# Kernel optimization log

Measured on AMD Instinct MI355X. Metric: run time of the kernel, lower is better.

The kernel has to match this reference:

```python
import jax, jax.numpy as jnp
import numpy as np

B, CIN, L, D, H, DK, DV, K, KE = 8, 16, 256, 256, 8, 32, 32, 3, 5
EPS = 1e-9

def r2c(p):
    return p[..., 0] + 1j * p[..., 1]

def c2r(z):
    return jnp.stack([jnp.real(z), jnp.imag(z)], axis=-1)

def conv1d(x, w):
    # x: [B,C,L] complex, w: [O,C,Kt] complex, 'same' padding (pad = K//2)
    kt = w.shape[-1]; pad = kt // 2; Lx = x.shape[-1]
    xp = jnp.pad(x, ((0, 0), (0, 0), (pad, pad)))
    return sum(jnp.einsum('bcl,oc->bol', xp[:, :, i:i + Lx], w[:, :, i]) for i in range(kt))

def eca(x, w):
    # Efficient Channel Attention (complex): global avg pool over length,
    # 1D conv (kernel KE) across channels, split sigmoid gate, rescale.
    C = x.shape[1]; pad = w.shape[0] // 2
    y = x.mean(axis=-1)                              # [B,C] complex
    yp = jnp.pad(y, ((0, 0), (pad, pad)))
    z = sum(w[i] * yp[:, i:i + C] for i in range(w.shape[0]))
    a = jax.nn.sigmoid(z.real) + 1j * jax.nn.sigmoid(z.imag)
    return x * a[:, :, None]

def magminmax(s):
    # MagMinMaxNorm: min-max normalize magnitudes along last dim, keep phase.
    mag = jnp.abs(s)
    mn = mag.min(axis=-1, keepdims=True)
    mx = mag.max(axis=-1, keepdims=True)
    return s * (((mag - mn) / (mx - mn + EPS)) / (mag + EPS))

def mha(qi, ki, vi, Wq, Wk, Wv, Wo):
    # qi/ki/vi: [B, L, D] complex
    b, lq, _ = qi.shape
    q = jnp.einsum('bld,de->ble', qi, Wq).reshape(b, lq, H, DK)
    k = jnp.einsum('bld,de->ble', ki, Wk).reshape(b, -1, H, DK)
    v = jnp.einsum('bld,de->ble', vi, Wv).reshape(b, -1, H, DV)
    s = jnp.einsum('bqhd,bkhd->bhqk', q, k) * (1.0 / DK ** 0.5)
    o = jnp.einsum('bhqk,bkhd->bqhd', magminmax(s), v).reshape(b, lq, H * DV)
    return jnp.einsum('ble,ed->bld', o, Wo)

def ssca(A, Bx, Wq, Wk, Wv, Wo, eca_w, conv_w):
    # A, Bx: [B, D, L] complex. Wq/Wk/Wv/Wo indexed [AA, BB, AB, BA].
    At = jnp.swapaxes(A, 1, 2)
    Bt = jnp.swapaxes(Bx, 1, 2)
    Waa = mha(At, At, At, Wq[0], Wk[0], Wv[0], Wo[0])
    Xbb = mha(Bt, Bt, Bt, Wq[1], Wk[1], Wv[1], Wo[1])
    Yab = mha(At, Bt, Bt, Wq[2], Wk[2], Wv[2], Wo[2])
    Zba = mha(Bt, At, At, Wq[3], Wk[3], Wv[3], Wo[3])
    # cat along sequence dim (dim=1 pre-transpose in torch), then back to [B, D, 4L]
    Xc = jnp.swapaxes(jnp.concatenate([Waa, Xbb, Yab, Zba], axis=1), 1, 2)
    return conv1d(eca(Xc, eca_w), conv_w)

def fusion(X1, X2, head_w, head_b, wq, wk, wv, wo, ssca_eca_w, ssca_conv_w, top_eca_w):
    X1c, X2c = r2c(X1), r2c(X2)
    hw, hb = r2c(head_w), r2c(head_b)
    Wq, Wk, Wv, Wo = r2c(wq), r2c(wk), r2c(wv), r2c(wo)
    se, sc, te = r2c(ssca_eca_w), r2c(ssca_conv_w), r2c(top_eca_w)
    A = conv1d(X1c, hw[0]) + hb[0][None, :, None]
    Bc = conv1d(X2c, hw[1]) + hb[1][None, :, None]
    R = ssca(A, Bc, Wq[0], Wk[0], Wv[0], Wo[0], se[0], sc[0])
    kk = ssca(jnp.fft.ifft(A, axis=-1), jnp.fft.ifft(Bc, axis=-1),
              Wq[1], Wk[1], Wv[1], Wo[1], se[1], sc[1])
    R2 = jnp.concatenate([R, jnp.fft.fft(kk, axis=-1)], axis=1)      # [B, 2D, 4L]
    k2 = jnp.concatenate([kk, jnp.fft.ifft(R2[:, :D], axis=-1)], axis=1)
    return eca(R2, te[0]), eca(k2, te[1])

def setup_inputs() -> dict:
    key = jax.random.key(0)
    ks = jax.random.split(key, 11)
    def rn(k, shape, s=1.0):
        return jax.random.normal(k, shape, dtype=jnp.float32) * s
    wscale = 1.0 / D ** 0.5
    return {
        'X1': rn(ks[0], (B, CIN, L, 2)),
        'X2': rn(ks[1], (B, CIN, L, 2)),
        'head_w': rn(ks[2], (2, D, CIN, K, 2), 0.1),
        'head_b': rn(ks[3], (2, D, 2), 0.1),
        'wq': rn(ks[4], (2, 4, D, H * DK, 2), wscale),
        'wk': rn(ks[5], (2, 4, D, H * DK, 2), wscale),
        'wv': rn(ks[6], (2, 4, D, H * DV, 2), wscale),
        'wo': rn(ks[7], (2, 4, H * DV, D, 2), wscale),
        'ssca_eca_w': rn(ks[8], (2, KE, 2), 0.3),
        'ssca_conv_w': rn(ks[9], (2, D, D, K, 2), wscale),
        'top_eca_w': rn(ks[10], (2, KE, 2), 0.3),
    }

def reference(X1, X2, head_w, head_b, wq, wk, wv, wo, ssca_eca_w, ssca_conv_w, top_eca_w):
    Rc, kc = fusion(X1, X2, head_w, head_b, wq, wk, wv, wo, ssca_eca_w, ssca_conv_w, top_eca_w)
    return c2r(Rc), c2r(kc)
```

## Files before the change

kernel.cpp:

```cpp
#include <hip/hip_runtime.h>
#include <math.h>

namespace {

constexpr int Bn = 8, CINn = 16, Ln = 256, Dn = 256, Hn = 8, DKn = 32, DVn = 32;
constexpr int KWn = 3, KEn = 5, L4n = 1024;
constexpr float EPSf = 1e-9f;
constexpr int XP = 1040;
constexpr int LP = 40;

typedef __attribute__((ext_vector_type(8))) short short8b;
typedef __attribute__((ext_vector_type(4))) float f32x4;

__device__ __forceinline__ float2 cmul(float2 a, float2 b){
  return make_float2(a.x*b.x - a.y*b.y, a.x*b.y + a.y*b.x);
}
__device__ __forceinline__ float2 cfma(float2 a, float2 b, float2 c){
  c.x = fmaf(a.x, b.x, c.x); c.x = fmaf(-a.y, b.y, c.x);
  c.y = fmaf(a.x, b.y, c.y); c.y = fmaf(a.y, b.x, c.y);
  return c;
}
__device__ __forceinline__ ushort f2bf(float f){
  uint u = __float_as_uint(f);
  u += 0x7fffu + ((u >> 16) & 1u);
  return (ushort)(u >> 16);
}
__device__ __forceinline__ short8b neg8(short8b v){
  union { short8b s; uint u[4]; } x; x.s = v;
  #pragma unroll
  for (int i = 0; i < 4; ++i) x.u[i] ^= 0x80008000u;
  return x.s;
}

__global__ void head_conv_kernel(const float2* __restrict__ X, const float2* __restrict__ hw,
                                 const float2* __restrict__ hb, float2* __restrict__ out){
  int idx = blockIdx.x * blockDim.x + threadIdx.x;
  if (idx >= Bn*Dn*Ln) return;
  int l = idx & (Ln-1);
  int o = (idx >> 8) & (Dn-1);
  int b = idx >> 16;
  float2 acc = hb[o];
  for (int c = 0; c < CINn; ++c){
    const float2* xr = X + (size_t)(b*CINn + c)*Ln;
    const float2* wr = hw + (size_t)(o*CINn + c)*KWn;
    #pragma unroll
    for (int i = 0; i < KWn; ++i){
      int ll = l + i - 1;
      if (ll >= 0 && ll < Ln) acc = cfma(xr[ll], wr[i], acc);
    }
  }
  out[idx] = acc;
}

template<int N, int LOG>
__global__ void fft_rows_kernel(const float2* __restrict__ src0, float2* __restrict__ dst0,
                                int schans, int scoff, int dchans, int dcoff,
                                float sign, float scale){
  __shared__ float2 buf[N];
  __shared__ float2 tw[N/2];
  int row = blockIdx.x;
  int rb = row >> 8, rc = row & 255;
  const float2* src = src0 + (size_t)(rb*schans + scoff + rc)*N;
  float2* dst = dst0 + (size_t)(rb*dchans + dcoff + rc)*N;
  int tid = threadIdx.x;
  for (int i = tid; i < N/2; i += 256){
    float a = sign * 6.2831853071795864f * (float)i / (float)N;
    float s, c; __sincosf(a, &s, &c);
    tw[i] = make_float2(c, s);
  }
  for (int i = tid; i < N; i += 256){
    unsigned r = __brev((unsigned)i) >> (32 - LOG);
    buf[r] = src[i];
  }
  __syncthreads();
  for (int st = 1; st <= LOG; ++st){
    int half = 1 << (st-1);
    for (int bf = tid; bf < N/2; bf += 256){
      int blk = bf >> (st-1);
      int pos = bf & (half-1);
      int i0 = (blk << st) + pos;
      int i1 = i0 + half;
      float2 w = tw[pos << (LOG-st)];
      float2 u = buf[i0];
      float2 t = cmul(w, buf[i1]);
      buf[i0] = make_float2(u.x + t.x, u.y + t.y);
      buf[i1] = make_float2(u.x - t.x, u.y - t.y);
    }
    __syncthreads();
  }
  for (int i = tid; i < N; i += 256)
    dst[i] = make_float2(buf[i].x * scale, buf[i].y * scale);
}

__device__ __forceinline__ void cgemm_core(
    const ushort* __restrict__ Are, const ushort* __restrict__ Aim, int pitchA, int am0,
    const ushort* __restrict__ Bre, const ushort* __restrict__ Bim, int pitchB, int n0,
    int K, int conv, float2* __restrict__ cbase, size_t crow, int cmode,
    ushort* __restrict__ ore, ushort* __restrict__ oim)
{
  __shared__ ushort sh[10240];
  ushort* As_re = sh;
  ushort* As_im = sh + 2560;
  ushort* Bs_re = sh + 5120;
  ushort* Bs_im = sh + 7680;
  int tid = threadIdx.x;
  int lane = tid & 63, w = tid >> 6;
  int wm = w >> 1, wn = w & 1;
  int lrow = lane & 15, lhalf = lane >> 4;
  f32x4 ar[2][2], ai[2][2];
  #pragma unroll
  for (int s = 0; s < 2; ++s)
    #pragma unroll
    for (int t = 0; t < 2; ++t){ ar[s][t] = (f32x4){0,0,0,0}; ai[s][t] = (f32x4){0,0,0,0}; }
  int nk = K >> 5;
  for (int kc = 0; kc < nk; ++kc){
    int k0 = kc << 5;
    __syncthreads();
    #pragma unroll
    for (int rep = 0; rep < 2; ++rep){
      int q = tid + rep*256;
      int row = q >> 3, kq = (q & 7)*4;
      size_t go = (size_t)(am0 + row)*pitchA + k0 + kq;
      *(uint2*)&As_re[row*LP + kq] = *(const uint2*)&Are[go];
      *(uint2*)&As_im[row*LP + kq] = *(const uint2*)&Aim[go];
    }
    if (!conv){
      #pragma unroll
      for (int rep = 0; rep < 2; ++rep){
        int q = tid + rep*256;
        int k = q >> 4, nq = (q & 15)*4;
        size_t go = (size_t)(k0 + k)*pitchB + n0 + nq;
        uint2 vr = *(const uint2*)&Bre[go];
        uint2 vi = *(const uint2*)&Bim[go];
        ushort* dr = &Bs_re[nq*LP + k];
        ushort* di = &Bs_im[nq*LP + k];
        dr[0]    = (ushort)(vr.x);      di[0]    = (ushort)(vi.x);
        dr[LP]   = (ushort)(vr.x>>16);  di[LP]   = (ushort)(vi.x>>16);
        dr[2*LP] = (ushort)(vr.y);      di[2*LP] = (ushort)(vi.y);
        dr[3*LP] = (ushort)(vr.y>>16);  di[3*LP] = (ushort)(vi.y>>16);
      }
    } else {
      #pragma unroll
      for (int rep = 0; rep < 8; ++rep){
        int idx = tid + rep*256;
        int k = idx >> 6, nn = idx & 63;
        uint kk = (uint)(k0 + k);
        uint c = (kk * 0xAAABu) >> 17;
        int i = (int)(kk - c*3u);
        size_t go = (size_t)c*XP + 8 + n0 + nn + i - 1;
        Bs_re[nn*LP + k] = Bre[go];
        Bs_im[nn*LP + k] = Bim[go];
      }
    }
    __syncthreads();
    short8b afr[2], afi[2], bfr[2], bfi[2];
    #pragma unroll
    for (int s = 0; s < 2; ++s){
      int row = wm*32 + s*16 + lrow;
      afr[s] = *(const short8b*)&As_re[row*LP + lhalf*8];
      afi[s] = *(const short8b*)&As_im[row*LP + lhalf*8];
    }
    #pragma unroll
    for (int t = 0; t < 2; ++t){
      int row = wn*32 + t*16 + lrow;
      bfr[t] = *(const short8b*)&Bs_re[row*LP + lhalf*8];
      bfi[t] = *(const short8b*)&Bs_im[row*LP + lhalf*8];
    }
    #pragma unroll
    for (int s = 0; s < 2; ++s){
      short8b ain = neg8(afi[s]);
      #pragma unroll
      for (int t = 0; t < 2; ++t){
        ar[s][t] = __builtin_amdgcn_mfma_f32_16x16x32_bf16(ain,    bfi[t], ar[s][t], 0, 0, 0);
        ar[s][t] = __builtin_amdgcn_mfma_f32_16x16x32_bf16(afr[s], bfr[t], ar[s][t], 0, 0, 0);
        ai[s][t] = __builtin_amdgcn_mfma_f32_16x16x32_bf16(afi[s], bfr[t], ai[s][t], 0, 0, 0);
        ai[s][t] = __builtin_amdgcn_mfma_f32_16x16x32_bf16(afr[s], bfi[t], ai[s][t], 0, 0, 0);
      }
    }
  }
  if (cmode == 0){
    #pragma unroll
    for (int s = 0; s < 2; ++s)
      #pragma unroll
      for (int t = 0; t < 2; ++t)
        #pragma unroll
        for (int r = 0; r < 4; ++r){
          int mm = wm*32 + s*16 + lhalf*4 + r;
          int nn = wn*32 + t*16 + lrow;
          if (ore){
            ore[(size_t)mm*crow + nn] = f2bf(ar[s][t][r]);
            oim[(size_t)mm*crow + nn] = f2bf(ai[s][t][r]);
          } else {
            cbase[(size_t)mm*crow + nn] = make_float2(ar[s][t][r], ai[s][t][r]);
          }
        }
  } else {
    float2* T = (float2*)sh;
    #pragma unroll
    for (int h2 = 0; h2 < 2; ++h2){
      __syncthreads();
      if (wn == h2){
        #pragma unroll
        for (int s = 0; s < 2; ++s)
          #pragma unroll
          for (int t = 0; t < 2; ++t)
            #pragma unroll
            for (int r = 0; r < 4; ++r){
              int mm = wm*32 + s*16 + lhalf*4 + r;
              int nn = t*16 + lrow;
              T[mm*33 + nn] = make_float2(ar[s][t][r], ai[s][t][r]);
            }
      }
      __syncthreads();
      #pragma unroll
      for (int rep = 0; rep < 8; ++rep){
        int idx = tid + rep*256;
        int mm = idx & 63, nn = idx >> 6;
        float2 v = T[mm*33 + nn];
        if (ore){
          ore[(size_t)(h2*32 + nn)*crow + mm] = f2bf(v.x);
          oim[(size_t)(h2*32 + nn)*crow + mm] = f2bf(v.y);
        } else {
          cbase[(size_t)(h2*32 + nn)*crow + mm] = v;
        }
      }
    }
  }
}

__global__ __launch_bounds__(256) void qkv_mfma(
    const ushort* __restrict__ aAre, const ushort* __restrict__ aAim,
    const ushort* __restrict__ aBre, const ushort* __restrict__ aBim,
    const ushort* __restrict__ WqRe, const ushort* __restrict__ WqIm,
    const ushort* __restrict__ WkRe, const ushort* __restrict__ WkIm,
    const ushort* __restrict__ WvRe, const ushort* __restrict__ WvIm,
    ushort* __restrict__ QpRe, ushort* __restrict__ QpIm,
    ushort* __restrict__ KpRe, ushort* __restrict__ KpIm,
    ushort* __restrict__ VpRe, ushort* __restrict__ VpIm,
    int set, int m0, size_t pstride)
{
  int my = blockIdx.y;
  int ml = my / 3, which = my - ml*3;
  int m = m0 + ml;
  bool useA = (which == 0) ? (m == 0 || m == 2) : (m == 0 || m == 3);
  const ushort* Are = useA ? aAre : aBre;
  const ushort* Aim = useA ? aAim : aBim;
  const ushort* WRe = (which == 0) ? WqRe : (which == 1) ? WkRe : WvRe;
  const ushort* WIm = (which == 0) ? WqIm : (which == 1) ? WkIm : WvIm;
  size_t woff = (size_t)(set*4 + m)*Dn*Dn;
  int bx = blockIdx.x;
  int nt = bx & 3, mt = (bx >> 2) & 3, b = bx >> 4;
  int l0 = mt*64, e0 = nt*64;
  const ushort* ARe = Are + (size_t)b*Ln*Dn;
  const ushort* AIm = Aim + (size_t)b*Ln*Dn;
  size_t po = (size_t)ml*pstride;
  if (which == 2){
    ushort* orp = VpRe + po + ((size_t)b*Dn + e0)*Ln + l0;
    ushort* oip = VpIm + po + ((size_t)b*Dn + e0)*Ln + l0;
    cgemm_core(ARe, AIm, Dn, l0, WRe + woff, WIm + woff, Dn, e0, Dn, 0,
               nullptr, Ln, 1, orp, oip);
  } else {
    ushort* orp = ((which == 0) ? QpRe : KpRe) + po + ((size_t)b*Ln + l0)*Dn + e0;
    ushort* oip = ((which == 0) ? QpIm : KpIm) + po + ((size_t)b*Ln + l0)*Dn + e0;
    cgemm_core(ARe, AIm, Dn, l0, WRe + woff, WIm + woff, Dn, e0, Dn, 0,
               nullptr, Dn, 0, orp, oip);
  }
}

__global__ __launch_bounds__(256) void wo_mfma(
    const ushort* __restrict__ ORe, const ushort* __restrict__ OIm,
    const ushort* __restrict__ WoRe, const ushort* __restrict__ WoIm,
    float2* __restrict__ Xc, int set, int m0)
{
  int ml = blockIdx.y;
  int m = m0 + ml;
  size_t woff = (size_t)(set*4 + m)*Dn*Dn;
  int bx = blockIdx.x;
  int nt = bx & 3, mt = (bx >> 2) & 3, b = bx >> 4;
  int l0 = mt*64, d0 = nt*64;
  const ushort* ARe = ORe + ((size_t)ml*Bn + b)*Ln*Dn;
  const ushort* AIm = OIm + ((size_t)ml*Bn + b)*Ln*Dn;
  float2* cb = Xc + ((size_t)b*Dn + d0)*L4n + m*Ln + l0;
  cgemm_core(ARe, AIm, Dn, l0, WoRe + woff, WoIm + woff, Dn, d0, Dn, 0,
             cb, L4n, 1, nullptr, nullptr);
}

__global__ __launch_bounds__(256) void conv_mfma(
    const ushort* __restrict__ WRe, const ushort* __restrict__ WIm,
    const ushort* __restrict__ XRe, const ushort* __restrict__ XIm,
    float2* __restrict__ out, int ochans)
{
  int bx = blockIdx.x;
  int xt = bx & 15, ot = (bx >> 4) & 3, b = bx >> 6;
  int o0 = ot*64, x0 = xt*64;
  const ushort* xr = XRe + (size_t)b*Dn*XP;
  const ushort* xi = XIm + (size_t)b*Dn*XP;
  float2* cb = out + ((size_t)(b*ochans) + o0)*L4n + x0;
  cgemm_core(WRe, WIm, 768, o0, xr, xi, XP, x0, 768, 1, cb, L4n, 0,
             nullptr, nullptr);
}

__global__ __launch_bounds__(256) void attn_mfma(
    const ushort* __restrict__ QRe, const ushort* __restrict__ QIm,
    const ushort* __restrict__ KRe, const ushort* __restrict__ KIm,
    const ushort* __restrict__ VRe, const ushort* __restrict__ VIm,
    ushort* __restrict__ ORe, ushort* __restrict__ OIm, size_t pstride)
{
  size_t po = (size_t)blockIdx.y*pstride;
  const ushort* qre = QRe + po; const ushort* qim = QIm + po;
  const ushort* kre = KRe + po; const ushort* kim = KIm + po;
  const ushort* vre = VRe + po; const ushort* vim = VIm + po;
  ushort* ore = ORe + po; ushort* oim = OIm + po;
  int bx = blockIdx.x;
  int qt = bx >> 6, h = (bx >> 3) & 7, b = bx & 7;
  int q0 = qt*16;
  int tid = threadIdx.x;
  int lane = tid & 63, w = tid >> 6;
  int lg = lane >> 4, lr = lane & 15;
  __shared__ ushort PsRe[16*264];
  __shared__ ushort PsIm[16*264];
  __shared__ float2 mmb[4][4][4];
  __shared__ float2 red[4][16][32];
  const float scl = 0.17677669529663687f;

  size_t qoff = ((size_t)(b*Ln + q0 + lr))*Dn + h*DKn + lg*8;
  short8b aqr = *(const short8b*)&qre[qoff];
  short8b aqi = *(const short8b*)&qim[qoff];
  short8b aqin = neg8(aqi);

  f32x4 sr[4], si[4];
  #pragma unroll
  for (int t = 0; t < 4; ++t){ sr[t] = (f32x4){0,0,0,0}; si[t] = (f32x4){0,0,0,0}; }
  #pragma unroll
  for (int t = 0; t < 4; ++t){
    int kcol = w*64 + t*16 + lr;
    size_t koff = ((size_t)(b*Ln + kcol))*Dn + h*DKn + lg*8;
    short8b bkr = *(const short8b*)&kre[koff];
    short8b bki = *(const short8b*)&kim[koff];
    sr[t] = __builtin_amdgcn_mfma_f32_16x16x32_bf16(aqin, bki, sr[t], 0, 0, 0);
    sr[t] = __builtin_amdgcn_mfma_f32_16x16x32_bf16(aqr,  bkr, sr[t], 0, 0, 0);
    si[t] = __builtin_amdgcn_mfma_f32_16x16x32_bf16(aqi,  bkr, si[t], 0, 0, 0);
    si[t] = __builtin_amdgcn_mfma_f32_16x16x32_bf16(aqr,  bki, si[t], 0, 0, 0);
  }
  float mag[4][4];
  float mnr[4], mxr[4];
  #pragma unroll
  for (int r = 0; r < 4; ++r){ mnr[r] = 3.4e38f; mxr[r] = 0.f; }
  #pragma unroll
  for (int t = 0; t < 4; ++t)
    #pragma unroll
    for (int r = 0; r < 4; ++r){
      float x = sr[t][r]*scl, y = si[t][r]*scl;
      sr[t][r] = x; si[t][r] = y;
      float m = sqrtf(x*x + y*y);
      mag[t][r] = m;
      mnr[r] = fminf(mnr[r], m); mxr[r] = fmaxf(mxr[r], m);
    }
  #pragma unroll
  for (int off = 1; off < 16; off <<= 1)
    #pragma unroll
    for (int r = 0; r < 4; ++r){
      mnr[r] = fminf(mnr[r], __shfl_xor(mnr[r], off));
      mxr[r] = fmaxf(mxr[r], __shfl_xor(mxr[r], off));
    }
  if (lr == 0){
    #pragma unroll
    for (int r = 0; r < 4; ++r) mmb[w][lg][r] = make_float2(mnr[r], mxr[r]);
  }
  __syncthreads();
  float fmn[4], fmx[4];
  #pragma unroll
  for (int r = 0; r < 4; ++r){
    float2 v0 = mmb[0][lg][r], v1 = mmb[1][lg][r];
    float2 v2 = mmb[2][lg][r], v3 = mmb[3][lg][r];
    fmn[r] = fminf(fminf(v0.x, v1.x), fminf(v2.x, v3.x));
    fmx[r] = fmaxf(fmaxf(v0.y, v1.y), fmaxf(v2.y, v3.y));
  }
  #pragma unroll
  for (int t = 0; t < 4; ++t)
    #pragma unroll
    for (int r = 0; r < 4; ++r){
      int q = lg*4 + r, k = w*64 + t*16 + lr;
      float m = mag[t][r];
      float f = ((m - fmn[r]) / (fmx[r] - fmn[r] + EPSf)) / (m + EPSf);
      PsRe[q*264 + k] = f2bf(sr[t][r]*f);
      PsIm[q*264 + k] = f2bf(si[t][r]*f);
    }
  __syncthreads();
  f32x4 pr[2], pi[2];
  #pragma unroll
  for (int t = 0; t < 2; ++t){ pr[t] = (f32x4){0,0,0,0}; pi[t] = (f32x4){0,0,0,0}; }
  #pragma unroll
  for (int kc = 0; kc < 2; ++kc){
    int k0 = w*64 + kc*32;
    short8b par = *(const short8b*)&PsRe[lr*264 + k0 + lg*8];
    short8b pai = *(const short8b*)&PsIm[lr*264 + k0 + lg*8];
    short8b pain = neg8(pai);
    #pragma unroll
    for (int t = 0; t < 2; ++t){
      int dv = t*16 + lr;
      size_t voff = ((size_t)(b*Dn + h*DVn + dv))*Ln + k0 + lg*8;
      short8b bvr = *(const short8b*)&vre[voff];
      short8b bvi = *(const short8b*)&vim[voff];
      pr[t] = __builtin_amdgcn_mfma_f32_16x16x32_bf16(pain, bvi, pr[t], 0, 0, 0);
      pr[t] = __builtin_amdgcn_mfma_f32_16x16x32_bf16(par,  bvr, pr[t], 0, 0, 0);
      pi[t] = __builtin_amdgcn_mfma_f32_16x16x32_bf16(pai,  bvr, pi[t], 0, 0, 0);
      pi[t] = __builtin_amdgcn_mfma_f32_16x16x32_bf16(par,  bvi, pi[t], 0, 0, 0);
    }
  }
  #pragma unroll
  for (int t = 0; t < 2; ++t)
    #pragma unroll
    for (int r = 0; r < 4; ++r)
      red[w][lg*4 + r][t*16 + lr] = make_float2(pr[t][r], pi[t][r]);
  __syncthreads();
  #pragma unroll
  for (int rep = 0; rep < 2; ++rep){
    int idx = tid + rep*256;
    int q = idx >> 5, dv = idx & 31;
    float2 s0 = red[0][q][dv], s1 = red[1][q][dv];
    float2 s2 = red[2][q][dv], s3 = red[3][q][dv];
    float sx = s0.x + s1.x + s2.x + s3.x;
    float sy = s0.y + s1.y + s2.y + s3.y;
    size_t oo = ((size_t)(b*Ln + q0 + q))*Dn + h*DVn + dv;
    ore[oo] = f2bf(sx); oim[oo] = f2bf(sy);
  }
}

__global__ void pack_at(const float2* __restrict__ in, ushort* __restrict__ ore,
                        ushort* __restrict__ oim){
  __shared__ float2 T[32][33];
  int bx = blockIdx.x;
  int lt = bx & 7, dt = (bx >> 3) & 7, b = bx >> 6;
  int tid = threadIdx.x;
  int c = tid & 31, rr = tid >> 5;
  #pragma unroll
  for (int it = 0; it < 4; ++it){
    int d = rr + it*8;
    T[d][c] = in[((size_t)b*Dn + dt*32 + d)*Ln + lt*32 + c];
  }
  __syncthreads();
  #pragma unroll
  for (int it = 0; it < 4; ++it){
    int l = rr + it*8;
    float2 v = T[c][l];
    size_t o = ((size_t)b*Ln + lt*32 + l)*Dn + dt*32 + c;
    ore[o] = f2bf(v.x); oim[o] = f2bf(v.y);
  }
}

__global__ void pack_w(const float2* __restrict__ wq, const float2* __restrict__ wk,
                       const float2* __restrict__ wv, const float2* __restrict__ wo,
                       ushort* r0, ushort* i0, ushort* r1, ushort* i1,
                       ushort* r2, ushort* i2, ushort* r3, ushort* i3){
  int f = blockIdx.y;
  const float2* in = (f == 0) ? wq : (f == 1) ? wk : (f == 2) ? wv : wo;
  ushort* orr = (f == 0) ? r0 : (f == 1) ? r1 : (f == 2) ? r2 : r3;
  ushort* oii = (f == 0) ? i0 : (f == 1) ? i1 : (f == 2) ? i2 : i3;
  size_t idx = (size_t)blockIdx.x*256 + threadIdx.x;
  float2 v = in[idx];
  orr[idx] = f2bf(v.x); oii[idx] = f2bf(v.y);
}

__global__ void pack_sc(const float2* __restrict__ sc, ushort* __restrict__ ore,
                        ushort* __restrict__ oim){
  size_t idx = (size_t)blockIdx.x*256 + threadIdx.x;
  float2 v = sc[idx];
  ore[idx] = f2bf(v.x); oim[idx] = f2bf(v.y);
}

__global__ void eca_apply_pack(const float2* __restrict__ X, const float2* __restrict__ g,
                               ushort* __restrict__ xre, ushort* __restrict__ xim){
  int idx = blockIdx.x*256 + threadIdx.x;
  int row = idx >> 10, x = idx & 1023;
  float2 v = cmul(X[idx], g[row]);
  size_t o = (size_t)row*XP + 8 + x;
  xre[o] = f2bf(v.x); xim[o] = f2bf(v.y);
  if (x < 8){ size_t o2 = (size_t)row*XP + x; xre[o2] = 0; xim[o2] = 0; }
  if (x >= 1016){ size_t o2 = (size_t)row*XP + x + 16; xre[o2] = 0; xim[o2] = 0; }
}

__global__ void row_mean_kernel(const float2* __restrict__ X, float2* __restrict__ y){
  int row = blockIdx.x;
  int tid = threadIdx.x;
  float sx = 0.f, sy = 0.f;
  const float2* xr = X + (size_t)row*L4n;
  for (int i = tid; i < L4n; i += 256){ float2 v = xr[i]; sx += v.x; sy += v.y; }
  __shared__ float rx[256], ry[256];
  rx[tid] = sx; ry[tid] = sy; __syncthreads();
  for (int st = 128; st > 0; st >>= 1){
    if (tid < st){ rx[tid] += rx[tid+st]; ry[tid] += ry[tid+st]; }
    __syncthreads();
  }
  if (tid == 0) y[row] = make_float2(rx[0]*(1.f/L4n), ry[0]*(1.f/L4n));
}

__global__ void eca_gate_kernel(const float2* __restrict__ y, const float2* __restrict__ w,
                                float2* __restrict__ g, int C){
  int idx = blockIdx.x*blockDim.x + threadIdx.x;
  if (idx >= Bn*C) return;
  int c = idx % C;
  int b = idx / C;
  float2 z = make_float2(0.f, 0.f);
  #pragma unroll
  for (int i = 0; i < KEn; ++i){
    int cc = c + i - 2;
    if (cc >= 0 && cc < C) z = cfma(w[i], y[b*C + cc], z);
  }
  g[idx] = make_float2(1.f/(1.f + expf(-z.x)), 1.f/(1.f + expf(-z.y)));
}

__global__ void eca_apply_kernel(float2* __restrict__ X, const float2* __restrict__ g){
  int idx = blockIdx.x*256 + threadIdx.x;
  int row = idx >> 10;
  X[idx] = cmul(X[idx], g[row]);
}

}

extern "C" void kernel_launch(void* const* d_in, const int* in_sizes, int n_in,
                              void* d_out, int out_size, void* d_ws, size_t ws_size,
                              hipStream_t stream){
  const float2* X1 = (const float2*)d_in[0];
  const float2* X2 = (const float2*)d_in[1];
  const float2* head_w = (const float2*)d_in[2];
  const float2* head_b = (const float2*)d_in[3];
  const float2* wq = (const float2*)d_in[4];
  const float2* wk = (const float2*)d_in[5];
  const float2* wv = (const float2*)d_in[6];
  const float2* wo = (const float2*)d_in[7];
  const float2* se = (const float2*)d_in[8];
  const float2* sc = (const float2*)d_in[9];
  const float2* te = (const float2*)d_in[10];

  const size_t SZ_BDL = (size_t)Bn*Dn*Ln;
  const size_t SZ_X   = (size_t)Bn*Dn*L4n;
  const size_t small  = 2*(size_t)Bn*2*Dn;
  const size_t NAt    = (size_t)Bn*Ln*Dn;

  const size_t US_FIX = 2*(4*NAt)
                      + 2*(4*8*(size_t)65536)
                      + 2*(2*(size_t)Dn*768)
                      + 2*((size_t)Bn*Dn*XP);
  auto need_bytes = [&](int mc){
    return ((size_t)4*SZ_BDL + SZ_X + small)*sizeof(float2)
         + (US_FIX + (size_t)8*mc*NAt)*sizeof(ushort);
  };
  int mcount = 1;
  if (ws_size >= need_bytes(4)) mcount = 4;
  else if (ws_size >= need_bytes(2)) mcount = 2;

  float2* p = (float2*)d_ws;
  float2* A  = p;  p += SZ_BDL;
  float2* Bc = p;  p += SZ_BDL;
  float2* iA = p;  p += SZ_BDL;
  float2* iB = p;  p += SZ_BDL;
  float2* Xc = p;  p += SZ_X;
  float2* ybuf = p; p += (size_t)Bn*2*Dn;
  float2* gbuf = p; p += (size_t)Bn*2*Dn;

  ushort* us = (ushort*)p;
  auto grab = [&](size_t n){ ushort* r = us; us += n; return r; };
  ushort *AtRe[4], *AtIm[4];
  for (int i = 0; i < 4; ++i){ AtRe[i] = grab(NAt); AtIm[i] = grab(NAt); }
  ushort *WRe4[4], *WIm4[4];
  for (int f = 0; f < 4; ++f){ WRe4[f] = grab(8*(size_t)65536); WIm4[f] = grab(8*(size_t)65536); }
  ushort* ScRe = grab(2*(size_t)Dn*768);
  ushort* ScIm = grab(2*(size_t)Dn*768);
  ushort* XRe = grab((size_t)Bn*Dn*XP);
  ushort* XIm = grab((size_t)Bn*Dn*XP);
  ushort* QpRe = grab((size_t)mcount*NAt);
  ushort* QpIm = grab((size_t)mcount*NAt);
  ushort* KpRe = grab((size_t)mcount*NAt);
  ushort* KpIm = grab((size_t)mcount*NAt);
  ushort* VpRe = grab((size_t)mcount*NAt);
  ushort* VpIm = grab((size_t)mcount*NAt);
  ushort* ObRe = grab((size_t)mcount*NAt);
  ushort* ObIm = grab((size_t)mcount*NAt);

  float2* out0 = (float2*)d_out;
  float2* out1 = out0 + (size_t)Bn*2*Dn*L4n;

  head_conv_kernel<<<(Bn*Dn*Ln)/256, 256, 0, stream>>>(X1, head_w, head_b, A);
  head_conv_kernel<<<(Bn*Dn*Ln)/256, 256, 0, stream>>>(
      X2, head_w + (size_t)Dn*CINn*KWn, head_b + Dn, Bc);

  fft_rows_kernel<256,8><<<Bn*Dn, 256, 0, stream>>>(A,  iA, 256,0,256,0, 1.0f, 1.0f/256.0f);
  fft_rows_kernel<256,8><<<Bn*Dn, 256, 0, stream>>>(Bc, iB, 256,0,256,0, 1.0f, 1.0f/256.0f);

  pack_at<<<512, 256, 0, stream>>>(A,  AtRe[0], AtIm[0]);
  pack_at<<<512, 256, 0, stream>>>(Bc, AtRe[1], AtIm[1]);
  pack_at<<<512, 256, 0, stream>>>(iA, AtRe[2], AtIm[2]);
  pack_at<<<512, 256, 0, stream>>>(iB, AtRe[3], AtIm[3]);
  pack_w<<<dim3(2048, 4), 256, 0, stream>>>(wq, wk, wv, wo,
      WRe4[0], WIm4[0], WRe4[1], WIm4[1], WRe4[2], WIm4[2], WRe4[3], WIm4[3]);
  pack_sc<<<1536, 256, 0, stream>>>(sc, ScRe, ScIm);

  auto run_ssca = [&](int ia, int ib, int set, float2* dstbase){
    for (int m0 = 0; m0 < 4; m0 += mcount){
      qkv_mfma<<<dim3(Bn*16, 3*mcount), 256, 0, stream>>>(
          AtRe[ia], AtIm[ia], AtRe[ib], AtIm[ib],
          WRe4[0], WIm4[0], WRe4[1], WIm4[1], WRe4[2], WIm4[2],
          QpRe, QpIm, KpRe, KpIm, VpRe, VpIm, set, m0, NAt);
      attn_mfma<<<dim3(Bn*Hn*16, mcount), 256, 0, stream>>>(
          QpRe, QpIm, KpRe, KpIm, VpRe, VpIm, ObRe, ObIm, NAt);
      wo_mfma<<<dim3(Bn*16, mcount), 256, 0, stream>>>(
          ObRe, ObIm, WRe4[3], WIm4[3], Xc, set, m0);
    }
    row_mean_kernel<<<Bn*Dn, 256, 0, stream>>>(Xc, ybuf);
    eca_gate_kernel<<<(Bn*Dn + 255)/256, 256, 0, stream>>>(ybuf, se + set*KEn, gbuf, Dn);
    eca_apply_pack<<<(int)(SZ_X/256), 256, 0, stream>>>(Xc, gbuf, XRe, XIm);
    conv_mfma<<<Bn*64, 256, 0, stream>>>(
        ScRe + (size_t)set*Dn*768, ScIm + (size_t)set*Dn*768, XRe, XIm, dstbase, 2*Dn);
  };

  run_ssca(0, 1, 0, out0);
  run_ssca(2, 3, 1, out1);

  fft_rows_kernel<1024,10><<<Bn*Dn, 256, 0, stream>>>(out1, out0, 2*Dn,0, 2*Dn,Dn, -1.0f, 1.0f);
  fft_rows_kernel<1024,10><<<Bn*Dn, 256, 0, stream>>>(out0, out1, 2*Dn,0, 2*Dn,Dn, 1.0f, 1.0f/1024.0f);

  for (int t = 0; t < 2; ++t){
    float2* op = (t == 0) ? out0 : out1;
    row_mean_kernel<<<Bn*2*Dn, 256, 0, stream>>>(op, ybuf);
    eca_gate_kernel<<<(Bn*2*Dn + 255)/256, 256, 0, stream>>>(ybuf, te + t*KEn, gbuf, 2*Dn);
    eca_apply_kernel<<<(Bn*2*Dn*L4n)/256, 256, 0, stream>>>(op, gbuf);
  }
}
```

Measured before the change: 437.5 us.

## Compute ECA means algebraically, retile complex GEMMs, transpose weights at pack time

```diff
diff --git a/kernel.cpp b/kernel.cpp
--- a/kernel.cpp
+++ b/kernel.cpp
@@ -24,6 +24,9 @@
   uint u = __float_as_uint(f);
   u += 0x7fffu + ((u >> 16) & 1u);
   return (ushort)(u >> 16);
+}
+__device__ __forceinline__ float bf2f(ushort u){
+  return __uint_as_float((uint)u << 16);
 }
 __device__ __forceinline__ short8b neg8(short8b v){
   union { short8b s; uint u[4]; } x; x.s = v;
@@ -55,9 +58,10 @@
 template<int N, int LOG>
 __global__ void fft_rows_kernel(const float2* __restrict__ src0, float2* __restrict__ dst0,
                                 int schans, int scoff, int dchans, int dcoff,
-                                float sign, float scale){
+                                float sign, float scale, float2* __restrict__ ysum){
   __shared__ float2 buf[N];
   __shared__ float2 tw[N/2];
+  __shared__ float rx[256], ry[256];
   int row = blockIdx.x;
   int rb = row >> 8, rc = row & 255;
   const float2* src = src0 + (size_t)(rb*schans + scoff + rc)*N;
@@ -88,8 +92,20 @@
     }
     __syncthreads();
   }
-  for (int i = tid; i < N; i += 256)
-    dst[i] = make_float2(buf[i].x * scale, buf[i].y * scale);
+  float sx = 0.f, sy = 0.f;
+  for (int i = tid; i < N; i += 256){
+    float2 o = make_float2(buf[i].x * scale, buf[i].y * scale);
+    dst[i] = o; sx += o.x; sy += o.y;
+  }
+  if (ysum){
+    rx[tid] = sx; ry[tid] = sy; __syncthreads();
+    for (int st = 128; st > 0; st >>= 1){
+      if (tid < st){ rx[tid] += rx[tid+st]; ry[tid] += ry[tid+st]; }
+      __syncthreads();
+    }
+    if (tid == 0)
+      ysum[(size_t)rb*dchans + dcoff + rc] = make_float2(rx[0]*(1.f/N), ry[0]*(1.f/N));
+  }
 }
 
 __device__ __forceinline__ void cgemm_core(
@@ -98,26 +114,25 @@
     int K, int conv, float2* __restrict__ cbase, size_t crow, int cmode,
     ushort* __restrict__ ore, ushort* __restrict__ oim)
 {
-  __shared__ ushort sh[10240];
+  __shared__ ushort sh[16896];
   ushort* As_re = sh;
-  ushort* As_im = sh + 2560;
-  ushort* Bs_re = sh + 5120;
-  ushort* Bs_im = sh + 7680;
+  ushort* As_im = sh + 5120;
+  ushort* Bs_re = sh + 10240;
+  ushort* Bs_im = sh + 12800;
   int tid = threadIdx.x;
   int lane = tid & 63, w = tid >> 6;
-  int wm = w >> 1, wn = w & 1;
   int lrow = lane & 15, lhalf = lane >> 4;
-  f32x4 ar[2][2], ai[2][2];
+  f32x4 ar[2][4], ai[2][4];
   #pragma unroll
   for (int s = 0; s < 2; ++s)
     #pragma unroll
-    for (int t = 0; t < 2; ++t){ ar[s][t] = (f32x4){0,0,0,0}; ai[s][t] = (f32x4){0,0,0,0}; }
+    for (int t = 0; t < 4; ++t){ ar[s][t] = (f32x4){0,0,0,0}; ai[s][t] = (f32x4){0,0,0,0}; }
   int nk = K >> 5;
   for (int kc = 0; kc < nk; ++kc){
     int k0 = kc << 5;
     __syncthreads();
     #pragma unroll
-    for (int rep = 0; rep < 2; ++rep){
+    for (int rep = 0; rep < 4; ++rep){
       int q = tid + rep*256;
       int row = q >> 3, kq = (q & 7)*4;
       size_t go = (size_t)(am0 + row)*pitchA + k0 + kq;
@@ -128,16 +143,10 @@
       #pragma unroll
       for (int rep = 0; rep < 2; ++rep){
         int q = tid + rep*256;
-        int k = q >> 4, nq = (q & 15)*4;
-        size_t go = (size_t)(k0 + k)*pitchB + n0 + nq;
-        uint2 vr = *(const uint2*)&Bre[go];
-        uint2 vi = *(const uint2*)&Bim[go];
-        ushort* dr = &Bs_re[nq*LP + k];
-        ushort* di = &Bs_im[nq*LP + k];
-        dr[0]    = (ushort)(vr.x);      di[0]    = (ushort)(vi.x);
-        dr[LP]   = (ushort)(vr.x>>16);  di[LP]   = (ushort)(vi.x>>16);
-        dr[2*LP] = (ushort)(vr.y);      di[2*LP] = (ushort)(vi.y);
-        dr[3*LP] = (ushort)(vr.y>>16);  di[3*LP] = (ushort)(vi.y>>16);
+        int row = q >> 3, kq = (q & 7)*4;
+        size_t go = (size_t)(n0 + row)*pitchB + k0 + kq;
+        *(uint2*)&Bs_re[row*LP + kq] = *(const uint2*)&Bre[go];
+        *(uint2*)&Bs_im[row*LP + kq] = *(const uint2*)&Bim[go];
       }
     } else {
       #pragma unroll
@@ -153,16 +162,16 @@
       }
     }
     __syncthreads();
-    short8b afr[2], afi[2], bfr[2], bfi[2];
+    short8b afr[2], afi[2], bfr[4], bfi[4];
     #pragma unroll
     for (int s = 0; s < 2; ++s){
-      int row = wm*32 + s*16 + lrow;
+      int row = w*32 + s*16 + lrow;
       afr[s] = *(const short8b*)&As_re[row*LP + lhalf*8];
       afi[s] = *(const short8b*)&As_im[row*LP + lhalf*8];
     }
     #pragma unroll
-    for (int t = 0; t < 2; ++t){
-      int row = wn*32 + t*16 + lrow;
+    for (int t = 0; t < 4; ++t){
+      int row = t*16 + lrow;
       bfr[t] = *(const short8b*)&Bs_re[row*LP + lhalf*8];
       bfi[t] = *(const short8b*)&Bs_im[row*LP + lhalf*8];
     }
@@ -170,7 +179,7 @@
     for (int s = 0; s < 2; ++s){
       short8b ain = neg8(afi[s]);
       #pragma unroll
-      for (int t = 0; t < 2; ++t){
+      for (int t = 0; t < 4; ++t){
         ar[s][t] = __builtin_amdgcn_mfma_f32_16x16x32_bf16(ain,    bfi[t], ar[s][t], 0, 0, 0);
         ar[s][t] = __builtin_amdgcn_mfma_f32_16x16x32_bf16(afr[s], bfr[t], ar[s][t], 0, 0, 0);
         ai[s][t] = __builtin_amdgcn_mfma_f32_16x16x32_bf16(afi[s], bfr[t], ai[s][t], 0, 0, 0);
@@ -182,11 +191,11 @@
     #pragma unroll
     for (int s = 0; s < 2; ++s)
       #pragma unroll
-      for (int t = 0; t < 2; ++t)
+      for (int t = 0; t < 4; ++t)
         #pragma unroll
         for (int r = 0; r < 4; ++r){
-          int mm = wm*32 + s*16 + lhalf*4 + r;
-          int nn = wn*32 + t*16 + lrow;
+          int mm = w*32 + s*16 + lhalf*4 + r;
+          int nn = t*16 + lrow;
           if (ore){
             ore[(size_t)mm*crow + nn] = f2bf(ar[s][t][r]);
             oim[(size_t)mm*crow + nn] = f2bf(ai[s][t][r]);
@@ -199,23 +208,23 @@
     #pragma unroll
     for (int h2 = 0; h2 < 2; ++h2){
       __syncthreads();
-      if (wn == h2){
+      #pragma unroll
+      for (int s = 0; s < 2; ++s)
         #pragma unroll
-        for (int s = 0; s < 2; ++s)
+        for (int t2 = 0; t2 < 2; ++t2){
+          int t = h2*2 + t2;
           #pragma unroll
-          for (int t = 0; t < 2; ++t)
-            #pragma unroll
-            for (int r = 0; r < 4; ++r){
-              int mm = wm*32 + s*16 + lhalf*4 + r;
-              int nn = t*16 + lrow;
-              T[mm*33 + nn] = make_float2(ar[s][t][r], ai[s][t][r]);
-            }
-      }
+          for (int r = 0; r < 4; ++r){
+            int mm = w*32 + s*16 + lhalf*4 + r;
+            int nn = t2*16 + lrow;
+            T[mm*33 + nn] = make_float2(ar[s][t][r], ai[s][t][r]);
+          }
+        }
       __syncthreads();
       #pragma unroll
-      for (int rep = 0; rep < 8; ++rep){
+      for (int rep = 0; rep < 16; ++rep){
         int idx = tid + rep*256;
-        int mm = idx & 63, nn = idx >> 6;
+        int mm = idx & 127, nn = idx >> 7;
         float2 v = T[mm*33 + nn];
         if (ore){
           ore[(size_t)(h2*32 + nn)*crow + mm] = f2bf(v.x);
@@ -249,8 +258,8 @@
   const ushort* WIm = (which == 0) ? WqIm : (which == 1) ? WkIm : WvIm;
   size_t woff = (size_t)(set*4 + m)*Dn*Dn;
   int bx = blockIdx.x;
-  int nt = bx & 3, mt = (bx >> 2) & 3, b = bx >> 4;
-  int l0 = mt*64, e0 = nt*64;
+  int nt = bx & 3, mt = (bx >> 2) & 1, b = bx >> 3;
+  int l0 = mt*128, e0 = nt*64;
   const ushort* ARe = Are + (size_t)b*Ln*Dn;
   const ushort* AIm = Aim + (size_t)b*Ln*Dn;
   size_t po = (size_t)ml*pstride;
@@ -276,8 +285,8 @@
   int m = m0 + ml;
   size_t woff = (size_t)(set*4 + m)*Dn*Dn;
   int bx = blockIdx.x;
-  int nt = bx & 3, mt = (bx >> 2) & 3, b = bx >> 4;
-  int l0 = mt*64, d0 = nt*64;
+  int nt = bx & 3, mt = (bx >> 2) & 1, b = bx >> 3;
+  int l0 = mt*128, d0 = nt*64;
   const ushort* ARe = ORe + ((size_t)ml*Bn + b)*Ln*Dn;
   const ushort* AIm = OIm + ((size_t)ml*Bn + b)*Ln*Dn;
   float2* cb = Xc + ((size_t)b*Dn + d0)*L4n + m*Ln + l0;
@@ -291,8 +300,8 @@
     float2* __restrict__ out, int ochans)
 {
   int bx = blockIdx.x;
-  int xt = bx & 15, ot = (bx >> 4) & 3, b = bx >> 6;
-  int o0 = ot*64, x0 = xt*64;
+  int xt = bx & 15, ot = (bx >> 4) & 1, b = bx >> 5;
+  int o0 = ot*128, x0 = xt*64;
   const ushort* xr = XRe + (size_t)b*Dn*XP;
   const ushort* xi = XIm + (size_t)b*Dn*XP;
   float2* cb = out + ((size_t)(b*ochans) + o0)*L4n + x0;
@@ -320,7 +329,7 @@
   __shared__ ushort PsRe[16*264];
   __shared__ ushort PsIm[16*264];
   __shared__ float2 mmb[4][4][4];
-  __shared__ float2 red[4][16][32];
+  __shared__ float2 redbuf[4][16][32];
   const float scl = 0.17677669529663687f;
 
   size_t qoff = ((size_t)(b*Ln + q0 + lr))*Dn + h*DKn + lg*8;
@@ -342,47 +351,49 @@
     si[t] = __builtin_amdgcn_mfma_f32_16x16x32_bf16(aqi,  bkr, si[t], 0, 0, 0);
     si[t] = __builtin_amdgcn_mfma_f32_16x16x32_bf16(aqr,  bki, si[t], 0, 0, 0);
   }
-  float mag[4][4];
-  float mnr[4], mxr[4];
-  #pragma unroll
-  for (int r = 0; r < 4; ++r){ mnr[r] = 3.4e38f; mxr[r] = 0.f; }
+  float s2a[4][4];
+  float mn2[4], mx2[4];
+  #pragma unroll
+  for (int r = 0; r < 4; ++r){ mn2[r] = 3.4e38f; mx2[r] = 0.f; }
   #pragma unroll
   for (int t = 0; t < 4; ++t)
     #pragma unroll
     for (int r = 0; r < 4; ++r){
       float x = sr[t][r]*scl, y = si[t][r]*scl;
       sr[t][r] = x; si[t][r] = y;
-      float m = sqrtf(x*x + y*y);
-      mag[t][r] = m;
-      mnr[r] = fminf(mnr[r], m); mxr[r] = fmaxf(mxr[r], m);
+      float s2 = fmaf(x, x, y*y);
+      s2a[t][r] = s2;
+      mn2[r] = fminf(mn2[r], s2); mx2[r] = fmaxf(mx2[r], s2);
     }
   #pragma unroll
   for (int off = 1; off < 16; off <<= 1)
     #pragma unroll
     for (int r = 0; r < 4; ++r){
-      mnr[r] = fminf(mnr[r], __shfl_xor(mnr[r], off));
-      mxr[r] = fmaxf(mxr[r], __shfl_xor(mxr[r], off));
+      mn2[r] = fminf(mn2[r], __shfl_xor(mn2[r], off));
+      mx2[r] = fmaxf(mx2[r], __shfl_xor(mx2[r], off));
     }
   if (lr == 0){
     #pragma unroll
-    for (int r = 0; r < 4; ++r) mmb[w][lg][r] = make_float2(mnr[r], mxr[r]);
+    for (int r = 0; r < 4; ++r) mmb[w][lg][r] = make_float2(mn2[r], mx2[r]);
   }
   __syncthreads();
-  float fmn[4], fmx[4];
+  float mnv[4], invr[4];
   #pragma unroll
   for (int r = 0; r < 4; ++r){
     float2 v0 = mmb[0][lg][r], v1 = mmb[1][lg][r];
     float2 v2 = mmb[2][lg][r], v3 = mmb[3][lg][r];
-    fmn[r] = fminf(fminf(v0.x, v1.x), fminf(v2.x, v3.x));
-    fmx[r] = fmaxf(fmaxf(v0.y, v1.y), fmaxf(v2.y, v3.y));
+    float fmn2 = fminf(fminf(v0.x, v1.x), fminf(v2.x, v3.x));
+    float fmx2 = fmaxf(fmaxf(v0.y, v1.y), fmaxf(v2.y, v3.y));
+    mnv[r] = sqrtf(fmn2);
+    invr[r] = __builtin_amdgcn_rcpf(sqrtf(fmx2) - mnv[r] + EPSf);
   }
   #pragma unroll
   for (int t = 0; t < 4; ++t)
     #pragma unroll
     for (int r = 0; r < 4; ++r){
       int q = lg*4 + r, k = w*64 + t*16 + lr;
-      float m = mag[t][r];
-      float f = ((m - fmn[r]) / (fmx[r] - fmn[r] + EPSf)) / (m + EPSf);
+      float m = sqrtf(s2a[t][r]);
+      float f = (m - mnv[r])*invr[r]*__builtin_amdgcn_rcpf(m + EPSf);
       PsRe[q*264 + k] = f2bf(sr[t][r]*f);
       PsIm[q*264 + k] = f2bf(si[t][r]*f);
     }
@@ -408,18 +419,19 @@
       pi[t] = __builtin_amdgcn_mfma_f32_16x16x32_bf16(par,  bvi, pi[t], 0, 0, 0);
     }
   }
+  __syncthreads();
   #pragma unroll
   for (int t = 0; t < 2; ++t)
     #pragma unroll
     for (int r = 0; r < 4; ++r)
-      red[w][lg*4 + r][t*16 + lr] = make_float2(pr[t][r], pi[t][r]);
+      redbuf[w][lg*4 + r][t*16 + lr] = make_float2(pr[t][r], pi[t][r]);
   __syncthreads();
   #pragma unroll
   for (int rep = 0; rep < 2; ++rep){
     int idx = tid + rep*256;
     int q = idx >> 5, dv = idx & 31;
-    float2 s0 = red[0][q][dv], s1 = red[1][q][dv];
-    float2 s2 = red[2][q][dv], s3 = red[3][q][dv];
+    float2 s0 = redbuf[0][q][dv], s1 = redbuf[1][q][dv];
+    float2 s2 = redbuf[2][q][dv], s3 = redbuf[3][q][dv];
     float sx = s0.x + s1.x + s2.x + s3.x;
     float sy = s0.y + s1.y + s2.y + s3.y;
     size_t oo = ((size_t)(b*Ln + q0 + q))*Dn + h*DVn + dv;
@@ -449,17 +461,33 @@
   }
 }
 
-__global__ void pack_w(const float2* __restrict__ wq, const float2* __restrict__ wk,
-                       const float2* __restrict__ wv, const float2* __restrict__ wo,
-                       ushort* r0, ushort* i0, ushort* r1, ushort* i1,
-                       ushort* r2, ushort* i2, ushort* r3, ushort* i3){
+__global__ void pack_wt(const float2* __restrict__ wq, const float2* __restrict__ wk,
+                        const float2* __restrict__ wv, const float2* __restrict__ wo,
+                        ushort* r0, ushort* i0, ushort* r1, ushort* i1,
+                        ushort* r2, ushort* i2, ushort* r3, ushort* i3){
   int f = blockIdx.y;
   const float2* in = (f == 0) ? wq : (f == 1) ? wk : (f == 2) ? wv : wo;
   ushort* orr = (f == 0) ? r0 : (f == 1) ? r1 : (f == 2) ? r2 : r3;
   ushort* oii = (f == 0) ? i0 : (f == 1) ? i1 : (f == 2) ? i2 : i3;
-  size_t idx = (size_t)blockIdx.x*256 + threadIdx.x;
-  float2 v = in[idx];
-  orr[idx] = f2bf(v.x); oii[idx] = f2bf(v.y);
+  int bx = blockIdx.x;
+  int tile = bx & 63, mat = bx >> 6;
+  int kt = tile & 7, nt = tile >> 3;
+  __shared__ float2 T[32][33];
+  int tid = threadIdx.x;
+  int c = tid & 31, rr = tid >> 5;
+  #pragma unroll
+  for (int it = 0; it < 4; ++it){
+    int k = rr + it*8;
+    T[k][c] = in[((size_t)(mat*256 + kt*32 + k))*256 + nt*32 + c];
+  }
+  __syncthreads();
+  #pragma unroll
+  for (int it = 0; it < 4; ++it){
+    int n = rr + it*8;
+    float2 v = T[c][n];
+    size_t o = ((size_t)(mat*256 + nt*32 + n))*256 + kt*32 + c;
+    orr[o] = f2bf(v.x); oii[o] = f2bf(v.y);
+  }
 }
 
 __global__ void pack_sc(const float2* __restrict__ sc, ushort* __restrict__ ore,
@@ -470,29 +498,93 @@
 }
 
 __global__ void eca_apply_pack(const float2* __restrict__ X, const float2* __restrict__ g,
-                               ushort* __restrict__ xre, ushort* __restrict__ xim){
-  int idx = blockIdx.x*256 + threadIdx.x;
+                               ushort* __restrict__ xre, ushort* __restrict__ xim,
+                               float2* __restrict__ Xsum, float2* __restrict__ Xe0,
+                               float2* __restrict__ Xe1){
+  __shared__ float rx[256], ry[256];
+  int tid = threadIdx.x;
+  int idx = blockIdx.x*256 + tid;
   int row = idx >> 10, x = idx & 1023;
   float2 v = cmul(X[idx], g[row]);
   size_t o = (size_t)row*XP + 8 + x;
   xre[o] = f2bf(v.x); xim[o] = f2bf(v.y);
   if (x < 8){ size_t o2 = (size_t)row*XP + x; xre[o2] = 0; xim[o2] = 0; }
   if (x >= 1016){ size_t o2 = (size_t)row*XP + x + 16; xre[o2] = 0; xim[o2] = 0; }
-}
-
-__global__ void row_mean_kernel(const float2* __restrict__ X, float2* __restrict__ y){
-  int row = blockIdx.x;
-  int tid = threadIdx.x;
-  float sx = 0.f, sy = 0.f;
-  const float2* xr = X + (size_t)row*L4n;
-  for (int i = tid; i < L4n; i += 256){ float2 v = xr[i]; sx += v.x; sy += v.y; }
-  __shared__ float rx[256], ry[256];
-  rx[tid] = sx; ry[tid] = sy; __syncthreads();
+  if (x == 0) Xe0[row] = v;
+  if (x == 1023) Xe1[row] = v;
+  rx[tid] = v.x; ry[tid] = v.y; __syncthreads();
   for (int st = 128; st > 0; st >>= 1){
     if (tid < st){ rx[tid] += rx[tid+st]; ry[tid] += ry[tid+st]; }
     __syncthreads();
   }
-  if (tid == 0) y[row] = make_float2(rx[0]*(1.f/L4n), ry[0]*(1.f/L4n));
+  if (tid == 0){
+    atomicAdd(&Xsum[row].x, rx[0]);
+    atomicAdd(&Xsum[row].y, ry[0]);
+  }
+}
+
+__global__ void omean_kernel(const ushort* __restrict__ ORe, const ushort* __restrict__ OIm,
+                             float2* __restrict__ mo){
+  int blk = blockIdx.x;
+  int ch = blockIdx.y;
+  int e = threadIdx.x;
+  const ushort* pr = ORe + (size_t)blk*65536 + ch*32*256 + e;
+  const ushort* pi = OIm + (size_t)blk*65536 + ch*32*256 + e;
+  float sx = 0.f, sy = 0.f;
+  #pragma unroll 8
+  for (int l = 0; l < 32; ++l){ sx += bf2f(pr[l*256]); sy += bf2f(pi[l*256]); }
+  atomicAdd(&mo[blk*256 + e].x, sx);
+  atomicAdd(&mo[blk*256 + e].y, sy);
+}
+
+__global__ void xcmean_gemv(const float2* __restrict__ mo,
+                            const ushort* __restrict__ WoTRe, const ushort* __restrict__ WoTIm,
+                            float2* __restrict__ ybufX, int set, int m0, int mcount){
+  __shared__ float2 ms[256];
+  int b = blockIdx.x;
+  int d = threadIdx.x;
+  float2 acc = make_float2(0.f, 0.f);
+  for (int ml = 0; ml < mcount; ++ml){
+    int m = m0 + ml;
+    __syncthreads();
+    ms[d] = mo[(ml*Bn + b)*256 + d];
+    __syncthreads();
+    const ushort* wr = WoTRe + ((size_t)((set*4 + m)*256 + d))*256;
+    const ushort* wi = WoTIm + ((size_t)((set*4 + m)*256 + d))*256;
+    for (int e8 = 0; e8 < 32; ++e8){
+      short8b vr = *(const short8b*)&wr[e8*8];
+      short8b vi = *(const short8b*)&wi[e8*8];
+      #pragma unroll
+      for (int j = 0; j < 8; ++j){
+        float2 wv = make_float2(bf2f((ushort)vr[j]), bf2f((ushort)vi[j]));
+        acc = cfma(ms[e8*8 + j], wv, acc);
+      }
+    }
+  }
+  float2 old = ybufX[b*256 + d];
+  ybufX[b*256 + d] = make_float2(old.x + acc.x*(1.f/1024.f), old.y + acc.y*(1.f/1024.f));
+}
+
+__global__ void conv_mean(const float2* __restrict__ Xsum, const float2* __restrict__ Xe0,
+                          const float2* __restrict__ Xe1, const float2* __restrict__ sc,
+                          float2* __restrict__ ydst, int set){
+  int b = blockIdx.x;
+  int o = threadIdx.x;
+  const float2* wb = sc + ((size_t)(set*Dn + o))*Dn*KWn;
+  const float2* xs = Xsum + b*256;
+  const float2* e0 = Xe0 + b*256;
+  const float2* e1 = Xe1 + b*256;
+  float2 acc = make_float2(0.f, 0.f);
+  for (int c = 0; c < 256; ++c){
+    float2 w0 = wb[c*3], w1 = wb[c*3+1], w2 = wb[c*3+2];
+    float2 S = xs[c];
+    acc = cfma(S, w1, acc);
+    float2 t0 = make_float2(S.x - e1[c].x, S.y - e1[c].y);
+    acc = cfma(t0, w0, acc);
+    float2 t2 = make_float2(S.x - e0[c].x, S.y - e0[c].y);
+    acc = cfma(t2, w2, acc);
+  }
+  ydst[b*2*Dn + o] = make_float2(acc.x*(1.f/1024.f), acc.y*(1.f/1024.f));
 }
 
 __global__ void eca_gate_kernel(const float2* __restrict__ y, const float2* __restrict__ w,
@@ -510,10 +602,14 @@
   g[idx] = make_float2(1.f/(1.f + expf(-z.x)), 1.f/(1.f + expf(-z.y)));
 }
 
-__global__ void eca_apply_kernel(float2* __restrict__ X, const float2* __restrict__ g){
+__global__ void eca_apply4(float4* __restrict__ X, const float2* __restrict__ g){
   int idx = blockIdx.x*256 + threadIdx.x;
-  int row = idx >> 10;
-  X[idx] = cmul(X[idx], g[row]);
+  int row = idx >> 9;
+  float2 gg = g[row];
+  float4 v = X[idx];
+  float2 a = cmul(make_float2(v.x, v.y), gg);
+  float2 b = cmul(make_float2(v.z, v.w), gg);
+  X[idx] = make_float4(a.x, a.y, b.x, b.y);
 }
 
 }
@@ -535,15 +631,12 @@
 
   const size_t SZ_BDL = (size_t)Bn*Dn*Ln;
   const size_t SZ_X   = (size_t)Bn*Dn*L4n;
-  const size_t small  = 2*(size_t)Bn*2*Dn;
   const size_t NAt    = (size_t)Bn*Ln*Dn;
 
-  const size_t US_FIX = 2*(4*NAt)
-                      + 2*(4*8*(size_t)65536)
-                      + 2*(2*(size_t)Dn*768)
-                      + 2*((size_t)Bn*Dn*XP);
+  const size_t US_FIX = 2*(4*NAt) + 2*(4*8*(size_t)65536)
+                      + 2*(2*(size_t)Dn*768) + 2*((size_t)Bn*Dn*XP);
   auto need_bytes = [&](int mc){
-    return ((size_t)4*SZ_BDL + SZ_X + small)*sizeof(float2)
+    return ((size_t)4*SZ_BDL + SZ_X + 32768 + (size_t)mc*2048)*sizeof(float2)
          + (US_FIX + (size_t)8*mc*NAt)*sizeof(ushort);
   };
   int mcount = 1;
@@ -556,8 +649,14 @@
   float2* iA = p;  p += SZ_BDL;
   float2* iB = p;  p += SZ_BDL;
   float2* Xc = p;  p += SZ_X;
-  float2* ybuf = p; p += (size_t)Bn*2*Dn;
-  float2* gbuf = p; p += (size_t)Bn*2*Dn;
+  float2* ybufX = p; p += (size_t)Bn*Dn;
+  float2* ybufR = p; p += (size_t)Bn*2*Dn;
+  float2* ybufK = p; p += (size_t)Bn*2*Dn;
+  float2* gbuf  = p; p += (size_t)Bn*2*Dn;
+  float2* Xsum  = p; p += (size_t)Bn*Dn;
+  float2* Xe0   = p; p += (size_t)Bn*Dn;
+  float2* Xe1   = p; p += (size_t)Bn*Dn;
+  float2* mo    = p; p += (size_t)mcount*Bn*Dn;
 
   ushort* us = (ushort*)p;
   auto grab = [&](size_t n){ ushort* r = us; us += n; return r; };
@@ -585,45 +684,48 @@
   head_conv_kernel<<<(Bn*Dn*Ln)/256, 256, 0, stream>>>(
       X2, head_w + (size_t)Dn*CINn*KWn, head_b + Dn, Bc);
 
-  fft_rows_kernel<256,8><<<Bn*Dn, 256, 0, stream>>>(A,  iA, 256,0,256,0, 1.0f, 1.0f/256.0f);
-  fft_rows_kernel<256,8><<<Bn*Dn, 256, 0, stream>>>(Bc, iB, 256,0,256,0, 1.0f, 1.0f/256.0f);
+  fft_rows_kernel<256,8><<<Bn*Dn, 256, 0, stream>>>(A,  iA, 256,0,256,0, 1.0f, 1.0f/256.0f, nullptr);
+  fft_rows_kernel<256,8><<<Bn*Dn, 256, 0, stream>>>(Bc, iB, 256,0,256,0, 1.0f, 1.0f/256.0f, nullptr);
 
   pack_at<<<512, 256, 0, stream>>>(A,  AtRe[0], AtIm[0]);
   pack_at<<<512, 256, 0, stream>>>(Bc, AtRe[1], AtIm[1]);
   pack_at<<<512, 256, 0, stream>>>(iA, AtRe[2], AtIm[2]);
   pack_at<<<512, 256, 0, stream>>>(iB, AtRe[3], AtIm[3]);
-  pack_w<<<dim3(2048, 4), 256, 0, stream>>>(wq, wk, wv, wo,
+  pack_wt<<<dim3(512, 4), 256, 0, stream>>>(wq, wk, wv, wo,
       WRe4[0], WIm4[0], WRe4[1], WIm4[1], WRe4[2], WIm4[2], WRe4[3], WIm4[3]);
   pack_sc<<<1536, 256, 0, stream>>>(sc, ScRe, ScIm);
 
-  auto run_ssca = [&](int ia, int ib, int set, float2* dstbase){
+  auto run_ssca = [&](int ia, int ib, int set, float2* dstbase, float2* ybufT){
+    hipMemsetAsync(ybufX, 0, (size_t)Bn*Dn*sizeof(float2), stream);
     for (int m0 = 0; m0 < 4; m0 += mcount){
-      qkv_mfma<<<dim3(Bn*16, 3*mcount), 256, 0, stream>>>(
+      qkv_mfma<<<dim3(64, 3*mcount), 256, 0, stream>>>(
           AtRe[ia], AtIm[ia], AtRe[ib], AtIm[ib],
           WRe4[0], WIm4[0], WRe4[1], WIm4[1], WRe4[2], WIm4[2],
           QpRe, QpIm, KpRe, KpIm, VpRe, VpIm, set, m0, NAt);
       attn_mfma<<<dim3(Bn*Hn*16, mcount), 256, 0, stream>>>(
           QpRe, QpIm, KpRe, KpIm, VpRe, VpIm, ObRe, ObIm, NAt);
-      wo_mfma<<<dim3(Bn*16, mcount), 256, 0, stream>>>(
+      wo_mfma<<<dim3(64, mcount), 256, 0, stream>>>(
           ObRe, ObIm, WRe4[3], WIm4[3], Xc, set, m0);
-    }
-    row_mean_kernel<<<Bn*Dn, 256, 0, stream>>>(Xc, ybuf);
-    eca_gate_kernel<<<(Bn*Dn + 255)/256, 256, 0, stream>>>(ybuf, se + set*KEn, gbuf, Dn);
-    eca_apply_pack<<<(int)(SZ_X/256), 256, 0, stream>>>(Xc, gbuf, XRe, XIm);
-    conv_mfma<<<Bn*64, 256, 0, stream>>>(
+      hipMemsetAsync(mo, 0, (size_t)mcount*Bn*Dn*sizeof(float2), stream);
+      omean_kernel<<<dim3(mcount*Bn, 8), 256, 0, stream>>>(ObRe, ObIm, mo);
+      xcmean_gemv<<<Bn, 256, 0, stream>>>(mo, WRe4[3], WIm4[3], ybufX, set, m0, mcount);
+    }
+    hipMemsetAsync(Xsum, 0, (size_t)Bn*Dn*sizeof(float2), stream);
+    eca_gate_kernel<<<(Bn*Dn + 255)/256, 256, 0, stream>>>(ybufX, se + set*KEn, gbuf, Dn);
+    eca_apply_pack<<<(int)(SZ_X/256), 256, 0, stream>>>(Xc, gbuf, XRe, XIm, Xsum, Xe0, Xe1);
+    conv_mean<<<Bn, 256, 0, stream>>>(Xsum, Xe0, Xe1, sc, ybufT, set);
+    conv_mfma<<<256, 256, 0, stream>>>(
         ScRe + (size_t)set*Dn*768, ScIm + (size_t)set*Dn*768, XRe, XIm, dstbase, 2*Dn);
   };
 
-  run_ssca(0, 1, 0, out0);
-  run_ssca(2, 3, 1, out1);
-
-  fft_rows_kernel<1024,10><<<Bn*Dn, 256, 0, stream>>>(out1, out0, 2*Dn,0, 2*Dn,Dn, -1.0f, 1.0f);
-  fft_rows_kernel<1024,10><<<Bn*Dn, 256, 0, stream>>>(out0, out1, 2*Dn,0, 2*Dn,Dn, 1.0f, 1.0f/1024.0f);
-
-  for (int t = 0; t < 2; ++t){
-    float2* op = (t == 0) ? out0 : out1;
-    row_mean_kernel<<<Bn*2*Dn, 256, 0, stream>>>(op, ybuf);
-    eca_gate_kernel<<<(Bn*2*Dn + 255)/256, 256, 0, stream>>>(ybuf, te + t*KEn, gbuf, 2*Dn);
-    eca_apply_kernel<<<(Bn*2*Dn*L4n)/256, 256, 0, stream>>>(op, gbuf);
-  }
-}
+  run_ssca(0, 1, 0, out0, ybufR);
+  run_ssca(2, 3, 1, out1, ybufK);
+
+  fft_rows_kernel<1024,10><<<Bn*Dn, 256, 0, stream>>>(out1, out0, 2*Dn,0, 2*Dn,Dn, -1.0f, 1.0f, ybufR);
+  fft_rows_kernel<1024,10><<<Bn*Dn, 256, 0, stream>>>(out0, out1, 2*Dn,0, 2*Dn,Dn, 1.0f, 1.0f/1024.0f, ybufK);
+
+  eca_gate_kernel<<<(Bn*2*Dn + 255)/256, 256, 0, stream>>>(ybufR, te, gbuf, 2*Dn);
+  eca_apply4<<<(int)((size_t)Bn*2*Dn*L4n/2/256), 256, 0, stream>>>((float4*)out0, gbuf);
+  eca_gate_kernel<<<(Bn*2*Dn + 255)/256, 256, 0, stream>>>(ybufK, te + KEn, gbuf, 2*Dn);
+  eca_apply4<<<(int)((size_t)Bn*2*Dn*L4n/2/256), 256, 0, stream>>>((float4*)out1, gbuf);
+}
```

After: 603.2 us. 1.38x slower.
